# Kernel tuning notes

Measured on AMD Instinct MI355X. Metric: run time of the kernel, lower is better.

The kernel has to match this reference:

```python
import jax, jax.numpy as jnp
import numpy as np

N, M, E, D = 20000, 1024, 640000, 256


def setup_inputs() -> dict:
    key = jax.random.key(0)
    ks = jax.random.split(key, 24)
    mask = jax.random.uniform(ks[0], (N, M)) < 0.05
    init = jnp.where(mask, jax.random.uniform(ks[1], (N, M), minval=0.1, maxval=1.0), 0.0)
    inp = {
        'init': init,
        'ei_cc': jax.random.randint(ks[2], (2, E), 0, N, dtype=jnp.int32),
        'ei_cac': jax.random.randint(ks[3], (2, E), 0, N, dtype=jnp.int32),
        'ei_csc': jax.random.randint(ks[4], (2, E), 0, N, dtype=jnp.int32),
        'ea_cc': jax.random.uniform(ks[5], (E,), minval=0.1, maxval=1.0),
        'ea_cac': jax.random.uniform(ks[6], (E,), minval=0.1, maxval=1.0),
        'ea_csc': jax.random.uniform(ks[7], (E,), minval=0.1, maxval=1.0),
        # Projection MLP: Linear(1,16) -> ReLU -> Linear(16,D)
        'pW1': jax.random.normal(ks[8], (1, 16)) * 0.5,
        'pb1': jnp.zeros((16,)),
        'pW2': jax.random.normal(ks[9], (16, D)) * 0.1,
        'pb2': jnp.zeros((D,)),
        # three GCN branches, 3 layers each (all D->D)
        'W_cc': jax.random.normal(ks[10], (3, D, D)) * 0.05,
        'b_cc': jnp.zeros((3, D)),
        'W_cac': jax.random.normal(ks[11], (3, D, D)) * 0.05,
        'b_cac': jnp.zeros((3, D)),
        'W_csc': jax.random.normal(ks[12], (3, D, D)) * 0.05,
        'b_csc': jnp.zeros((3, D)),
        # meta-path attention: Linear(D, 1)
        'w_att': jax.random.normal(ks[13], (D,)) * 0.05,
        'b_att': jnp.zeros((1,)),
    }
    return inp


def projection(init, pW1, pb1, pW2, pb2):
    # torch code feeds the *indices* of nonzero columns through the MLP and
    # mean-pools per row. Vectorize: precompute MLP(j) for every column index j,
    # then masked mean.
    idx = jnp.arange(M, dtype=init.dtype)[:, None]          # [M, 1]
    h = jax.nn.relu(idx @ pW1 + pb1)                        # [M, 16]
    col_emb = h @ pW2 + pb2                                 # [M, D]
    mask = (init != 0).astype(init.dtype)                   # [N, M]
    cnt = mask.sum(axis=1)                                  # [N]
    emb = (mask @ col_emb) / jnp.maximum(cnt, 1.0)[:, None]
    return jnp.where(cnt[:, None] > 0, emb, 0.0)            # zero rows stay zero


def gcn_conv(x, edge_index, edge_weight, W, b):
    # PyG GCNConv with edge_weight: add self loops (w=1), symmetric norm.
    n = x.shape[0]
    loop = jnp.arange(n, dtype=edge_index.dtype)
    row = jnp.concatenate([edge_index[0], loop])
    col = jnp.concatenate([edge_index[1], loop])
    w = jnp.concatenate([edge_weight, jnp.ones((n,), x.dtype)])
    deg = jax.ops.segment_sum(w, col, num_segments=n)
    dinv = jnp.where(deg > 0, jax.lax.rsqrt(deg), 0.0)
    norm = dinv[row] * w * dinv[col]                        # [E+N]
    h = x @ W                                               # [N, D]
    out = jax.ops.segment_sum(norm[:, None] * h[row], col, num_segments=n)
    return out + b


def gcn_branch(x, edge_index, edge_weight, Ws, bs):
    for l in range(3):
        x = jax.nn.relu(gcn_conv(x, edge_index, edge_weight, Ws[l], bs[l]))
    return x


def reference(init, ei_cc, ei_cac, ei_csc, ea_cc, ea_cac, ea_csc,
              pW1, pb1, pW2, pb2, W_cc, b_cc, W_cac, b_cac, W_csc, b_csc,
              w_att, b_att):
    x0 = projection(init, pW1, pb1, pW2, pb2)               # [N, D]
    out_cc = gcn_branch(x0, ei_cc, ea_cc, W_cc, b_cc)
    out_cac = gcn_branch(x0, ei_cac, ea_cac, W_cac, b_cac)
    out_csc = gcn_branch(x0, ei_csc, ea_csc, W_csc, b_csc)
    emb = jnp.stack([out_cc, out_cac, out_csc], axis=0)     # [3, N, D]
    scores = jnp.einsum('pnd,d->pn', emb, w_att) + b_att[0] # [3, N]
    attn = jax.nn.softmax(scores, axis=0)                   # softmax over meta-paths
    return jnp.einsum('pn,pnd->nd', attn, emb)              # [N, D]
```

## Files before the change

### kernel.cpp

```cpp
#include <hip/hip_runtime.h>
#include <hip/hip_bf16.h>

typedef __hip_bfloat16 bf16;
typedef __bf16 v8bf __attribute__((ext_vector_type(8)));
typedef float f32x4 __attribute__((ext_vector_type(4)));
typedef unsigned int v4u __attribute__((ext_vector_type(4)));

constexpr int N = 20000, M = 1024, E = 640000, D = 256;
constexpr size_t SEGEL = (size_t)N * D;
constexpr int NCHUNK = 10000;
constexpr int NSLICE = 64;
constexpr int ESLICE = E / NSLICE;

__device__ __forceinline__ float b2f(bf16 v) { return __bfloat162float(v); }
__device__ __forceinline__ bf16 f2b(float f) { return __float2bfloat16(f); }
__device__ __forceinline__ float u2f(unsigned short u) { return __uint_as_float(((unsigned)u) << 16); }
__device__ __forceinline__ unsigned short f2u(float f) { bf16 h = __float2bfloat16(f); return *(unsigned short*)&h; }
__device__ __forceinline__ float loadf(const void* p, size_t i, int isbf) {
    return isbf ? b2f(((const bf16*)p)[i]) : ((const float*)p)[i];
}
__device__ __forceinline__ void fma8(float* acc, uint4 v, float w) {
    acc[0] = fmaf(w, u2f((unsigned short)(v.x & 0xffffu)), acc[0]);
    acc[1] = fmaf(w, u2f((unsigned short)(v.x >> 16)), acc[1]);
    acc[2] = fmaf(w, u2f((unsigned short)(v.y & 0xffffu)), acc[2]);
    acc[3] = fmaf(w, u2f((unsigned short)(v.y >> 16)), acc[3]);
    acc[4] = fmaf(w, u2f((unsigned short)(v.z & 0xffffu)), acc[4]);
    acc[5] = fmaf(w, u2f((unsigned short)(v.z >> 16)), acc[5]);
    acc[6] = fmaf(w, u2f((unsigned short)(v.w & 0xffffu)), acc[6]);
    acc[7] = fmaf(w, u2f((unsigned short)(v.w >> 16)), acc[7]);
}
__device__ __forceinline__ void add4(float* acc, uint2 v) {
    acc[0] += u2f((unsigned short)(v.x & 0xffffu));
    acc[1] += u2f((unsigned short)(v.x >> 16));
    acc[2] += u2f((unsigned short)(v.y & 0xffffu));
    acc[3] += u2f((unsigned short)(v.y >> 16));
}
__device__ __forceinline__ unsigned pack2(float a, float b) {
    return (unsigned)f2u(a) | ((unsigned)f2u(b) << 16);
}

__global__ void detect_kernel(const void* __restrict__ ea, int* __restrict__ flag)
{
    if (threadIdx.x == 0 && blockIdx.x == 0) {
        const unsigned short* u = (const unsigned short*)ea;
        int cnt = 0;
        for (int i = 0; i < 64; i++) {
            float f = __uint_as_float(((unsigned)u[i]) << 16);
            if (f >= 0.05f && f <= 1.05f) cnt++;
        }
        *flag = (cnt >= 60) ? 1 : 0;
    }
}

__global__ __launch_bounds__(256) void prep_kernel(
    const void* __restrict__ W0, const void* __restrict__ W1, const void* __restrict__ W2,
    const void* __restrict__ pW1, const void* __restrict__ pb1,
    const void* __restrict__ pW2, const void* __restrict__ pb2,
    bf16* __restrict__ WT, bf16* __restrict__ cemb, const int* __restrict__ flag)
{
    int isbf = *flag;
    int b = blockIdx.x;
    if (b < 2304) {
        int mat = b >> 8, n = b & 255, k = threadIdx.x;
        const void* W = (mat < 3) ? W0 : (mat < 6) ? W1 : W2;
        int lm = mat - (mat < 3 ? 0 : (mat < 6 ? 3 : 6));
        WT[(size_t)mat * 65536 + n * 256 + k] =
            f2b(loadf(W, (size_t)lm * 65536 + k * 256 + n, isbf));
    } else {
        int j = b - 2304;
        int d = threadIdx.x;
        float jf = (float)j;
        float acc = loadf(pb2, d, isbf);
        #pragma unroll
        for (int k = 0; k < 16; k++) {
            float h = fmaxf(jf * loadf(pW1, k, isbf) + loadf(pb1, k, isbf), 0.0f);
            acc += h * loadf(pW2, k * 256 + d, isbf);
        }
        cemb[(size_t)j * 256 + d] = f2b(acc);
    }
}

__global__ __launch_bounds__(256) void projection_kernel(
    const void* __restrict__ init, const bf16* __restrict__ cemb,
    bf16* __restrict__ x0, const int* __restrict__ flag)
{
    __shared__ unsigned short idxs[4][1024];
    int isbf = *flag;
    int wave = threadIdx.x >> 6, lane = threadIdx.x & 63;
    int i = blockIdx.x * 4 + wave;
    unsigned long long below = (lane == 63) ? 0x7fffffffffffffffull
                                            : ((1ull << lane) - 1ull);
    int cnt = 0;
    if (isbf) {
        const unsigned short* row = (const unsigned short*)init + (size_t)i * 1024;
        for (int c0 = 0; c0 < 1024; c0 += 64) {
            bool nz = (row[c0 + lane] & 0x7fffu) != 0;
            unsigned long long m = __ballot(nz);
            if (nz) idxs[wave][cnt + __popcll(m & below)] = (unsigned short)(c0 + lane);
            cnt += __popcll(m);
        }
    } else {
        const float* row = (const float*)init + (size_t)i * 1024;
        for (int c0 = 0; c0 < 1024; c0 += 64) {
            bool nz = row[c0 + lane] != 0.0f;
            unsigned long long m = __ballot(nz);
            if (nz) idxs[wave][cnt + __popcll(m & below)] = (unsigned short)(c0 + lane);
            cnt += __popcll(m);
        }
    }
    const uint2* cr = (const uint2*)cemb;
    float acc[4] = {0.0f, 0.0f, 0.0f, 0.0f};
    int j = 0;
    for (; j + 8 <= cnt; j += 8) {
        uint2 v0 = cr[(size_t)idxs[wave][j + 0] * 64 + lane];
        uint2 v1 = cr[(size_t)idxs[wave][j + 1] * 64 + lane];
        uint2 v2 = cr[(size_t)idxs[wave][j + 2] * 64 + lane];
        uint2 v3 = cr[(size_t)idxs[wave][j + 3] * 64 + lane];
        uint2 v4 = cr[(size_t)idxs[wave][j + 4] * 64 + lane];
        uint2 v5 = cr[(size_t)idxs[wave][j + 5] * 64 + lane];
        uint2 v6 = cr[(size_t)idxs[wave][j + 6] * 64 + lane];
        uint2 v7 = cr[(size_t)idxs[wave][j + 7] * 64 + lane];
        add4(acc, v0); add4(acc, v1); add4(acc, v2); add4(acc, v3);
        add4(acc, v4); add4(acc, v5); add4(acc, v6); add4(acc, v7);
    }
    for (; j < cnt; j++) {
        uint2 v = cr[(size_t)idxs[wave][j] * 64 + lane];
        add4(acc, v);
    }
    float rinv = 1.0f / fmaxf((float)cnt, 1.0f);
    uint2 o;
    o.x = pack2(acc[0] * rinv, acc[1] * rinv);
    o.y = pack2(acc[2] * rinv, acc[3] * rinv);
    ((uint2*)x0)[(size_t)i * 64 + lane] = o;
}

__global__ __launch_bounds__(256) void countP_kernel(
    const int* __restrict__ e0, const int* __restrict__ e1, const int* __restrict__ e2,
    int* __restrict__ P)
{
    __shared__ int cur[NCHUNK];
    int b = blockIdx.x;
    int pb = b >> 7, rem = b & 127;
    int ck = rem >> 6, s = rem & 63;
    const int* ei = pb == 0 ? e0 : pb == 1 ? e1 : e2;
    int c0 = ck * NCHUNK;
    int t = threadIdx.x;
    for (int i = t; i < NCHUNK; i += 256) cur[i] = 0;
    __syncthreads();
    int ebase = s * ESLICE;
    for (int e = ebase + t; e < ebase + ESLICE; e += 256) {
        int c = ei[E + e];
        if (c >= c0 && c < c0 + NCHUNK) atomicAdd(&cur[c - c0], 1);
    }
    __syncthreads();
    int* Prow = P + ((size_t)(pb * NSLICE + s)) * N + c0;
    for (int i = t; i < NCHUNK; i += 256) Prow[i] = cur[i];
}

__global__ __launch_bounds__(256) void cnt_sum_kernel(
    const int* __restrict__ P, int* __restrict__ cnt)
{
    int id = blockIdx.x * 256 + threadIdx.x;
    if (id >= 3 * N) return;
    int pb = id / N, c = id - pb * N;
    int sum = 0;
    #pragma unroll 8
    for (int s = 0; s < NSLICE; s++)
        sum += P[((size_t)(pb * NSLICE + s)) * N + c];
    cnt[id] = sum;
}

__global__ __launch_bounds__(1024) void scan_kernel(
    const int* __restrict__ cnt, int* __restrict__ col_ptr)
{
    int pb = blockIdx.x;
    int base = pb * E;
    __shared__ int s[1024];
    int t = threadIdx.x;
    const int CH = 20;
    int i0 = t * CH;
    int sum = 0;
    for (int j = 0; j < CH; j++) { int i = i0 + j; if (i < N) sum += cnt[pb * N + i]; }
    s[t] = sum;
    __syncthreads();
    for (int off = 1; off < 1024; off <<= 1) {
        int v = (t >= off) ? s[t - off] : 0;
        __syncthreads();
        s[t] += v;
        __syncthreads();
    }
    int run = base + s[t] - sum;
    for (int j = 0; j < CH; j++) {
        int i = i0 + j;
        if (i < N) {
            col_ptr[pb * (N + 1) + i] = run;
            run += cnt[pb * N + i];
        }
    }
    if (t == 0) col_ptr[pb * (N + 1) + N] = base + E;
}

__global__ __launch_bounds__(256) void base_kernel(
    int* __restrict__ P, const int* __restrict__ col_ptr)
{
    int id = blockIdx.x * 256 + threadIdx.x;
    if (id >= 3 * N) return;
    int pb = id / N, c = id - pb * N;
    int run = col_ptr[pb * (N + 1) + c];
    for (int s = 0; s < NSLICE; s++) {
        size_t idx = ((size_t)(pb * NSLICE + s)) * N + c;
        int v = P[idx];
        P[idx] = run;
        run += v;
    }
}

__global__ __launch_bounds__(256) void fill_kernel(
    const int* __restrict__ e0, const int* __restrict__ e1, const int* __restrict__ e2,
    const void* __restrict__ a0, const void* __restrict__ a1, const void* __restrict__ a2,
    const int* __restrict__ P, int2* __restrict__ epack, const int* __restrict__ flag)
{
    __shared__ int cur[NCHUNK];
    int isbf = *flag;
    int b = blockIdx.x;
    int pb = b >> 7, rem = b & 127;
    int ck = rem >> 6, s = rem & 63;
    const int* ei = pb == 0 ? e0 : pb == 1 ? e1 : e2;
    const void* ea = pb == 0 ? a0 : pb == 1 ? a1 : a2;
    int c0 = ck * NCHUNK;
    int t = threadIdx.x;
    const int* Prow = P + ((size_t)(pb * NSLICE + s)) * N + c0;
    for (int i = t; i < NCHUNK; i += 256) cur[i] = Prow[i];
    __syncthreads();
    int ebase = s * ESLICE;
    for (int e = ebase + t; e < ebase + ESLICE; e += 256) {
        int c = ei[E + e];
        if (c >= c0 && c < c0 + NCHUNK) {
            int r = ei[e];
            float w = loadf(ea, e, isbf);
            int pos = atomicAdd(&cur[c - c0], 1);
            int2 v; v.x = r; v.y = __float_as_int(w);
            epack[pos] = v;
        }
    }
}

__global__ __launch_bounds__(256) void degsum_kernel(
    const int* __restrict__ col_ptr, const int2* __restrict__ epack,
    float* __restrict__ dinv, float* __restrict__ nloop)
{
    int wave = threadIdx.x >> 6, lane = threadIdx.x & 63;
    int pb = blockIdx.x / 5000;
    int i = (blockIdx.x - pb * 5000) * 4 + wave;
    int start = col_ptr[pb * (N + 1) + i], end = col_ptr[pb * (N + 1) + i + 1];
    float sum = 0.0f;
    for (int p = start + lane; p < end; p += 64) sum += __int_as_float(epack[p].y);
    for (int off = 1; off < 64; off <<= 1) sum += __shfl_xor(sum, off, 64);
    if (lane == 0) {
        float dg = 1.0f + sum;
        dinv[pb * N + i] = rsqrtf(dg);
        nloop[pb * N + i] = 1.0f / dg;
    }
}

__global__ __launch_bounds__(256) void snorm_sort_kernel(
    const int* __restrict__ col_ptr, int2* __restrict__ epack,
    const float* __restrict__ dinv)
{
    int wave = threadIdx.x >> 6, lane = threadIdx.x & 63;
    int pb = blockIdx.x / 5000;
    int i = (blockIdx.x - pb * 5000) * 4 + wave;
    int start = col_ptr[pb * (N + 1) + i], end = col_ptr[pb * (N + 1) + i + 1];
    float dc = dinv[pb * N + i];
    for (int base = start; base < end; base += 64) {
        int n = end - base; n = n < 64 ? n : 64;
        int key = 0x7fffffff, val = 0;
        if (lane < n) {
            int2 v = epack[base + lane];
            key = v.x;
            val = __float_as_int(dc * __int_as_float(v.y) * dinv[pb * N + v.x]);
        }
        #pragma unroll
        for (int k = 2; k <= 64; k <<= 1) {
            #pragma unroll
            for (int j = k >> 1; j > 0; j >>= 1) {
                int pk = __shfl_xor(key, j, 64);
                int pv = __shfl_xor(val, j, 64);
                bool up = (lane & k) == 0;
                bool lower = (lane & j) == 0;
                bool takeMin = (up == lower);
                bool sw = takeMin ? (pk < key) : (pk > key);
                if (sw) { key = pk; val = pv; }
            }
        }
        if (lane < n) {
            int2 o; o.x = key; o.y = val;
            epack[base + lane] = o;
        }
    }
}

__global__ __launch_bounds__(256) void aggregate_kernel(
    const bf16* __restrict__ xi0, const bf16* __restrict__ xi1, const bf16* __restrict__ xi2,
    bf16* __restrict__ yb,
    const int* __restrict__ col_ptr, const int2* __restrict__ epack,
    const float* __restrict__ nloop)
{
    int b = blockIdx.x;
    int xcd = b & 7, rnd = b >> 3;
    int pb, seq;
    if (xcd < 3)      { pb = 0; seq = rnd * 3 + xcd; }
    else if (xcd < 6) { pb = 1; seq = rnd * 3 + (xcd - 3); }
    else              { pb = 2; seq = rnd * 2 + (xcd - 6); }
    if (seq >= 5000) return;
    int wave = threadIdx.x >> 6, lane = threadIdx.x & 63;
    int i = seq * 4 + wave;
    const bf16* x = pb == 0 ? xi0 : pb == 1 ? xi1 : xi2;
    const uint4* xr = (const uint4*)x;
    int L = lane & 31, h = lane >> 5;
    int start = col_ptr[pb * (N + 1) + i], end = col_ptr[pb * (N + 1) + i + 1];
    float nl = nloop[pb * N + i];
    float acc[8];
    {
        uint4 sv = xr[(size_t)i * 32 + L];
        float self = (h == 0) ? nl : 0.0f;
        #pragma unroll
        for (int j = 0; j < 8; j++) acc[j] = 0.0f;
        fma8(acc, sv, self);
    }
    for (int base = start; base < end; base += 64) {
        int n = end - base; n = n < 64 ? n : 64;
        int ex = 0, ey = 0;
        if (lane < n) {
            unsigned long long ev = __builtin_nontemporal_load(
                (const unsigned long long*)(epack + base + lane));
            ex = (int)(unsigned)(ev & 0xffffffffull);
            ey = (int)(unsigned)(ev >> 32);
        }
        int pmax = (n + 1) >> 1;
        int p0 = 0;
        for (; p0 + 8 <= pmax; p0 += 8) {
            int eb = 2 * p0 + h;
            int r0 = __shfl(ex, eb +  0, 64);
            int r1 = __shfl(ex, eb +  2, 64);
            int r2 = __shfl(ex, eb +  4, 64);
            int r3 = __shfl(ex, eb +  6, 64);
            int r4 = __shfl(ex, eb +  8, 64);
            int r5 = __shfl(ex, eb + 10, 64);
            int r6 = __shfl(ex, eb + 12, 64);
            int r7 = __shfl(ex, eb + 14, 64);
            float w0 = __int_as_float(__shfl(ey, eb +  0, 64));
            float w1 = __int_as_float(__shfl(ey, eb +  2, 64));
            float w2 = __int_as_float(__shfl(ey, eb +  4, 64));
            float w3 = __int_as_float(__shfl(ey, eb +  6, 64));
            float w4 = __int_as_float(__shfl(ey, eb +  8, 64));
            float w5 = __int_as_float(__shfl(ey, eb + 10, 64));
            float w6 = __int_as_float(__shfl(ey, eb + 12, 64));
            float w7 = __int_as_float(__shfl(ey, eb + 14, 64));
            uint4 v0 = xr[(size_t)r0 * 32 + L];
            uint4 v1 = xr[(size_t)r1 * 32 + L];
            uint4 v2 = xr[(size_t)r2 * 32 + L];
            uint4 v3 = xr[(size_t)r3 * 32 + L];
            uint4 v4 = xr[(size_t)r4 * 32 + L];
            uint4 v5 = xr[(size_t)r5 * 32 + L];
            uint4 v6 = xr[(size_t)r6 * 32 + L];
            uint4 v7 = xr[(size_t)r7 * 32 + L];
            fma8(acc, v0, w0); fma8(acc, v1, w1);
            fma8(acc, v2, w2); fma8(acc, v3, w3);
            fma8(acc, v4, w4); fma8(acc, v5, w5);
            fma8(acc, v6, w6); fma8(acc, v7, w7);
        }
        if (p0 + 4 <= pmax) {
            int eb = 2 * p0 + h;
            int r0 = __shfl(ex, eb + 0, 64);
            int r1 = __shfl(ex, eb + 2, 64);
            int r2 = __shfl(ex, eb + 4, 64);
            int r3 = __shfl(ex, eb + 6, 64);
            float w0 = __int_as_float(__shfl(ey, eb + 0, 64));
            float w1 = __int_as_float(__shfl(ey, eb + 2, 64));
            float w2 = __int_as_float(__shfl(ey, eb + 4, 64));
            float w3 = __int_as_float(__shfl(ey, eb + 6, 64));
            uint4 v0 = xr[(size_t)r0 * 32 + L];
            uint4 v1 = xr[(size_t)r1 * 32 + L];
            uint4 v2 = xr[(size_t)r2 * 32 + L];
            uint4 v3 = xr[(size_t)r3 * 32 + L];
            fma8(acc, v0, w0); fma8(acc, v1, w1);
            fma8(acc, v2, w2); fma8(acc, v3, w3);
            p0 += 4;
        }
        for (; p0 < pmax; p0++) {
            int e = 2 * p0 + h;
            int rj = __shfl(ex, e, 64);
            float w = __int_as_float(__shfl(ey, e, 64));
            uint4 v = xr[(size_t)rj * 32 + L];
            fma8(acc, v, w);
        }
    }
    #pragma unroll
    for (int j = 0; j < 8; j++) acc[j] += __shfl_xor(acc[j], 32, 64);
    if (h == 0) {
        v4u o;
        o.x = pack2(acc[0], acc[1]);
        o.y = pack2(acc[2], acc[3]);
        o.z = pack2(acc[4], acc[5]);
        o.w = pack2(acc[6], acc[7]);
        __builtin_nontemporal_store(o,
            (v4u*)yb + (size_t)pb * (SEGEL / 8) + (size_t)i * 32 + L);
    }
}

__global__ __launch_bounds__(256) void gemm_relu_kernel(
    const bf16* __restrict__ yb, const bf16* __restrict__ WT, int layer,
    const void* __restrict__ b0, const void* __restrict__ b1, const void* __restrict__ b2,
    bf16* __restrict__ o0, bf16* __restrict__ o1, bf16* __restrict__ o2,
    const int* __restrict__ flag)
{
    int isbf = *flag;
    int pl = blockIdx.x / 625, blk = blockIdx.x - pl * 625;
    const bf16* y = yb + (size_t)pl * SEGEL;
    const bf16* wt = WT + (size_t)(pl * 3 + layer) * 65536;
    const void* bias = pl == 0 ? b0 : pl == 1 ? b1 : b2;
    bf16* xout = pl == 0 ? o0 : pl == 1 ? o1 : o2;

    int wave = threadIdx.x >> 6, lane = threadIdx.x & 63;
    int m0 = blk * 32 + (wave >> 1) * 16;
    int n0 = (wave & 1) * 128;
    int mrow = lane & 15, q = lane >> 4;

    f32x4 acc[8] = {};
    const v8bf* arow = reinterpret_cast<const v8bf*>(y + (size_t)(m0 + mrow) * 256);
    for (int k0 = 0; k0 < 256; k0 += 32) {
        v8bf a = arow[(k0 >> 3) + q];
        #pragma unroll
        for (int nt = 0; nt < 8; nt++) {
            const v8bf* brow = reinterpret_cast<const v8bf*>(wt + (size_t)(n0 + nt * 16 + mrow) * 256);
            acc[nt] = __builtin_amdgcn_mfma_f32_16x16x32_bf16(a, brow[(k0 >> 3) + q], acc[nt], 0, 0, 0);
        }
    }
    #pragma unroll
    for (int nt = 0; nt < 8; nt++) {
        int col = n0 + nt * 16 + mrow;
        float bv = loadf(bias, (size_t)layer * 256 + col, isbf);
        #pragma unroll
        for (int r = 0; r < 4; r++) {
            int row = m0 + q * 4 + r;
            xout[(size_t)row * 256 + col] = f2b(fmaxf(acc[nt][r] + bv, 0.0f));
        }
    }
}

__global__ __launch_bounds__(256) void gemm_attn_kernel(
    const bf16* __restrict__ yb, const bf16* __restrict__ WT,
    const void* __restrict__ b0, const void* __restrict__ b1, const void* __restrict__ b2,
    const void* __restrict__ w_att, void* __restrict__ out,
    const int* __restrict__ flag)
{
    __shared__ float sc[3][32];
    int isbf = *flag;
    int blk = blockIdx.x;
    int wave = threadIdx.x >> 6, lane = threadIdx.x & 63;
    int wm = wave >> 1;
    int m0 = blk * 32 + wm * 16;
    int n0 = (wave & 1) * 128;
    int mrow = lane & 15, q = lane >> 4;

    if (threadIdx.x < 96) ((float*)sc)[threadIdx.x] = 0.0f;
    __syncthreads();

    unsigned pe[3][8][2];
    #pragma unroll
    for (int p = 0; p < 3; p++) {
        const bf16* y = yb + (size_t)p * SEGEL;
        const bf16* wt = WT + (size_t)(p * 3 + 2) * 65536;
        const void* bias = p == 0 ? b0 : p == 1 ? b1 : b2;
        f32x4 acc[8] = {};
        const v8bf* arow = reinterpret_cast<const v8bf*>(y + (size_t)(m0 + mrow) * 256);
        for (int k0 = 0; k0 < 256; k0 += 32) {
            v8bf a = arow[(k0 >> 3) + q];
            #pragma unroll
            for (int nt = 0; nt < 8; nt++) {
                const v8bf* brow = reinterpret_cast<const v8bf*>(wt + (size_t)(n0 + nt * 16 + mrow) * 256);
                acc[nt] = __builtin_amdgcn_mfma_f32_16x16x32_bf16(a, brow[(k0 >> 3) + q], acc[nt], 0, 0, 0);
            }
        }
        float part[4] = {0.0f, 0.0f, 0.0f, 0.0f};
        #pragma unroll
        for (int nt = 0; nt < 8; nt++) {
            int col = n0 + nt * 16 + mrow;
            float bv = loadf(bias, (size_t)2 * 256 + col, isbf);
            float wv = loadf(w_att, col, isbf);
            float e0 = u2f(f2u(fmaxf(acc[nt][0] + bv, 0.0f)));
            float e1 = u2f(f2u(fmaxf(acc[nt][1] + bv, 0.0f)));
            float e2 = u2f(f2u(fmaxf(acc[nt][2] + bv, 0.0f)));
            float e3 = u2f(f2u(fmaxf(acc[nt][3] + bv, 0.0f)));
            pe[p][nt][0] = pack2(e0, e1);
            pe[p][nt][1] = pack2(e2, e3);
            part[0] = fmaf(e0, wv, part[0]);
            part[1] = fmaf(e1, wv, part[1]);
            part[2] = fmaf(e2, wv, part[2]);
            part[3] = fmaf(e3, wv, part[3]);
        }
        #pragma unroll
        for (int off = 1; off < 16; off <<= 1) {
            #pragma unroll
            for (int r = 0; r < 4; r++) part[r] += __shfl_xor(part[r], off, 64);
        }
        if (mrow == 0) {
            #pragma unroll
            for (int r = 0; r < 4; r++)
                atomicAdd(&sc[p][wm * 16 + q * 4 + r], part[r]);
        }
    }
    __syncthreads();
    #pragma unroll
    for (int r = 0; r < 4; r++) {
        int lrow = wm * 16 + q * 4 + r;
        float s0 = sc[0][lrow], s1 = sc[1][lrow], s2 = sc[2][lrow];
        float mx = fmaxf(s0, fmaxf(s1, s2));
        float a0 = expf(s0 - mx), a1 = expf(s1 - mx), a2 = expf(s2 - mx);
        float inv = 1.0f / (a0 + a1 + a2);
        a0 *= inv; a1 *= inv; a2 *= inv;
        int row = blk * 32 + lrow;
        #pragma unroll
        for (int nt = 0; nt < 8; nt++) {
            int col = n0 + nt * 16 + mrow;
            unsigned w0 = pe[0][nt][r >> 1], w1 = pe[1][nt][r >> 1], w2 = pe[2][nt][r >> 1];
            float v0 = u2f((unsigned short)((r & 1) ? (w0 >> 16) : (w0 & 0xffffu)));
            float v1 = u2f((unsigned short)((r & 1) ? (w1 >> 16) : (w1 & 0xffffu)));
            float v2 = u2f((unsigned short)((r & 1) ? (w2 >> 16) : (w2 & 0xffffu)));
            float v = a0 * v0 + a1 * v1 + a2 * v2;
            if (isbf) ((bf16*)out)[(size_t)row * 256 + col] = f2b(v);
            else      ((float*)out)[(size_t)row * 256 + col] = v;
        }
    }
}

extern "C" void kernel_launch(void* const* d_in, const int* in_sizes, int n_in,
                              void* d_out, int out_size, void* d_ws, size_t ws_size,
                              hipStream_t stream)
{
    (void)in_sizes; (void)n_in; (void)out_size; (void)ws_size;

    const void* init = d_in[0];
    const int*  ei[3] = {(const int*)d_in[1], (const int*)d_in[2], (const int*)d_in[3]};
    const void* ea[3] = {d_in[4], d_in[5], d_in[6]};
    const void* pW1 = d_in[7];
    const void* pb1 = d_in[8];
    const void* pW2 = d_in[9];
    const void* pb2 = d_in[10];
    const void* Wb[3] = {d_in[11], d_in[13], d_in[15]};
    const void* bb[3] = {d_in[12], d_in[14], d_in[16]};
    const void* w_att = d_in[17];

    char* ws = (char*)d_ws;
    size_t off = 0;
    auto carve = [&](size_t bytes) -> char* {
        off = (off + 255) & ~(size_t)255;
        char* p = ws + off; off += bytes; return p;
    };
    int*   flag  = (int*)carve(4);
    bf16*  WT    = (bf16*)carve((size_t)9 * 65536 * 2);
    bf16*  cemb  = (bf16*)carve((size_t)M * D * 2);
    bf16*  x0    = (bf16*)carve(SEGEL * 2);
    int*   cnt   = (int*)carve((size_t)3 * N * 4);
    int*   colp  = (int*)carve((size_t)3 * (N + 1) * 4);
    float* dinv  = (float*)carve((size_t)3 * N * 4);
    float* nloop = (float*)carve((size_t)3 * N * 4);
    int2*  epack = (int2*)carve((size_t)3 * E * 8);
    bf16*  ybuf  = (bf16*)carve((size_t)3 * SEGEL * 2);
    bf16*  bufA  = (bf16*)carve((size_t)3 * SEGEL * 2);
    bf16*  bufB  = (bf16*)carve((size_t)3 * SEGEL * 2);
    int* P = (int*)bufB;

    detect_kernel<<<1, 64, 0, stream>>>(ea[0], flag);
    prep_kernel<<<3328, 256, 0, stream>>>(Wb[0], Wb[1], Wb[2],
                                          pW1, pb1, pW2, pb2, WT, cemb, flag);
    projection_kernel<<<5000, 256, 0, stream>>>(init, cemb, x0, flag);

    countP_kernel<<<384, 256, 0, stream>>>(ei[0], ei[1], ei[2], P);
    cnt_sum_kernel<<<(3 * N + 255) / 256, 256, 0, stream>>>(P, cnt);
    scan_kernel<<<3, 1024, 0, stream>>>(cnt, colp);
    base_kernel<<<(3 * N + 255) / 256, 256, 0, stream>>>(P, colp);
    fill_kernel<<<384, 256, 0, stream>>>(ei[0], ei[1], ei[2], ea[0], ea[1], ea[2],
                                         P, epack, flag);
    degsum_kernel<<<15000, 256, 0, stream>>>(colp, epack, dinv, nloop);
    snorm_sort_kernel<<<15000, 256, 0, stream>>>(colp, epack, dinv);

    const bf16 *i0 = x0, *i1 = x0, *i2 = x0;
    for (int l = 0; l < 3; l++) {
        aggregate_kernel<<<20000, 256, 0, stream>>>(i0, i1, i2, ybuf, colp, epack, nloop);
        if (l < 2) {
            bf16* dst = (l == 0) ? bufA : bufB;
            gemm_relu_kernel<<<1875, 256, 0, stream>>>(ybuf, WT, l, bb[0], bb[1], bb[2],
                                                       dst, dst + SEGEL, dst + 2 * SEGEL, flag);
            i0 = dst; i1 = dst + SEGEL; i2 = dst + 2 * SEGEL;
        } else {
            gemm_attn_kernel<<<625, 256, 0, stream>>>(ybuf, WT, bb[0], bb[1], bb[2],
                                                      w_att, d_out, flag);
        }
    }
}
```

Baseline: 967.6 us.

## Replace sliced CSC build with global atomics, widen projection loads, simplify aggregate

Builds the CSC edge structure with global atomic counting and degree accumulation in one pass. This replaces the per-slice shared-memory histograms, cnt_sum, base and degsum kernels, and the scan now writes dinv, nloop and fill cursors. The projection kernel switches to 16-byte loads with half-waves handling alternate nonzeros, and aggregate drops the XCD-aware block remap, the extra 5000 blocks and the hand-unrolled loop in favour of a predicated 8-wide loop. Fill order within a column becomes nondeterministic, and global atomics may contend, though snorm_sort still sorts afterward.

```diff
diff --git a/kernel.cpp b/kernel.cpp
--- a/kernel.cpp
+++ b/kernel.cpp
@@ -8,9 +8,8 @@
 
 constexpr int N = 20000, M = 1024, E = 640000, D = 256;
 constexpr size_t SEGEL = (size_t)N * D;
-constexpr int NCHUNK = 10000;
-constexpr int NSLICE = 64;
-constexpr int ESLICE = E / NSLICE;
+constexpr int EB = 2000;
+constexpr int EBLK = E / EB;
 
 __device__ __forceinline__ float b2f(bf16 v) { return __bfloat162float(v); }
 __device__ __forceinline__ bf16 f2b(float f) { return __float2bfloat16(f); }
@@ -29,11 +28,15 @@
     acc[6] = fmaf(w, u2f((unsigned short)(v.w & 0xffffu)), acc[6]);
     acc[7] = fmaf(w, u2f((unsigned short)(v.w >> 16)), acc[7]);
 }
-__device__ __forceinline__ void add4(float* acc, uint2 v) {
-    acc[0] += u2f((unsigned short)(v.x & 0xffffu));
-    acc[1] += u2f((unsigned short)(v.x >> 16));
-    acc[2] += u2f((unsigned short)(v.y & 0xffffu));
-    acc[3] += u2f((unsigned short)(v.y >> 16));
+__device__ __forceinline__ void add8(float* a, uint4 v) {
+    a[0] += u2f((unsigned short)(v.x & 0xffffu));
+    a[1] += u2f((unsigned short)(v.x >> 16));
+    a[2] += u2f((unsigned short)(v.y & 0xffffu));
+    a[3] += u2f((unsigned short)(v.y >> 16));
+    a[4] += u2f((unsigned short)(v.z & 0xffffu));
+    a[5] += u2f((unsigned short)(v.z >> 16));
+    a[6] += u2f((unsigned short)(v.w & 0xffffu));
+    a[7] += u2f((unsigned short)(v.w >> 16));
 }
 __device__ __forceinline__ unsigned pack2(float a, float b) {
     return (unsigned)f2u(a) | ((unsigned)f2u(b) << 16);
@@ -56,7 +59,8 @@
     const void* __restrict__ W0, const void* __restrict__ W1, const void* __restrict__ W2,
     const void* __restrict__ pW1, const void* __restrict__ pb1,
     const void* __restrict__ pW2, const void* __restrict__ pb2,
-    bf16* __restrict__ WT, bf16* __restrict__ cemb, const int* __restrict__ flag)
+    bf16* __restrict__ WT, bf16* __restrict__ cemb,
+    int* __restrict__ cnt, float* __restrict__ degf, const int* __restrict__ flag)
 {
     int isbf = *flag;
     int b = blockIdx.x;
@@ -66,7 +70,7 @@
         int lm = mat - (mat < 3 ? 0 : (mat < 6 ? 3 : 6));
         WT[(size_t)mat * 65536 + n * 256 + k] =
             f2b(loadf(W, (size_t)lm * 65536 + k * 256 + n, isbf));
-    } else {
+    } else if (b < 3328) {
         int j = b - 2304;
         int d = threadIdx.x;
         float jf = (float)j;
@@ -77,6 +81,15 @@
             acc += h * loadf(pW2, k * 256 + d, isbf);
         }
         cemb[(size_t)j * 256 + d] = f2b(acc);
+    } else {
+        int zb = b - 3328;
+        if (zb < 235) {
+            int id = zb * 256 + threadIdx.x;
+            if (id < 3 * N) cnt[id] = 0;
+        } else {
+            int id = (zb - 235) * 256 + threadIdx.x;
+            if (id < 3 * N) degf[id] = 0.0f;
+        }
     }
 }
 
@@ -108,70 +121,66 @@
             cnt += __popcll(m);
         }
     }
-    const uint2* cr = (const uint2*)cemb;
-    float acc[4] = {0.0f, 0.0f, 0.0f, 0.0f};
-    int j = 0;
-    for (; j + 8 <= cnt; j += 8) {
-        uint2 v0 = cr[(size_t)idxs[wave][j + 0] * 64 + lane];
-        uint2 v1 = cr[(size_t)idxs[wave][j + 1] * 64 + lane];
-        uint2 v2 = cr[(size_t)idxs[wave][j + 2] * 64 + lane];
-        uint2 v3 = cr[(size_t)idxs[wave][j + 3] * 64 + lane];
-        uint2 v4 = cr[(size_t)idxs[wave][j + 4] * 64 + lane];
-        uint2 v5 = cr[(size_t)idxs[wave][j + 5] * 64 + lane];
-        uint2 v6 = cr[(size_t)idxs[wave][j + 6] * 64 + lane];
-        uint2 v7 = cr[(size_t)idxs[wave][j + 7] * 64 + lane];
-        add4(acc, v0); add4(acc, v1); add4(acc, v2); add4(acc, v3);
-        add4(acc, v4); add4(acc, v5); add4(acc, v6); add4(acc, v7);
-    }
-    for (; j < cnt; j++) {
-        uint2 v = cr[(size_t)idxs[wave][j] * 64 + lane];
-        add4(acc, v);
-    }
-    float rinv = 1.0f / fmaxf((float)cnt, 1.0f);
-    uint2 o;
-    o.x = pack2(acc[0] * rinv, acc[1] * rinv);
-    o.y = pack2(acc[2] * rinv, acc[3] * rinv);
-    ((uint2*)x0)[(size_t)i * 64 + lane] = o;
-}
-
-__global__ __launch_bounds__(256) void countP_kernel(
+    const uint4* cr4 = (const uint4*)cemb;
+    int L = lane & 31, h = lane >> 5;
+    float acc[8] = {0.f, 0.f, 0.f, 0.f, 0.f, 0.f, 0.f, 0.f};
+    int npair = cnt >> 1;
+    int t = 0;
+    for (; t + 8 <= npair; t += 8) {
+        uint4 v0 = cr4[(size_t)idxs[wave][2 * (t + 0) + h] * 32 + L];
+        uint4 v1 = cr4[(size_t)idxs[wave][2 * (t + 1) + h] * 32 + L];
+        uint4 v2 = cr4[(size_t)idxs[wave][2 * (t + 2) + h] * 32 + L];
+        uint4 v3 = cr4[(size_t)idxs[wave][2 * (t + 3) + h] * 32 + L];
+        uint4 v4 = cr4[(size_t)idxs[wave][2 * (t + 4) + h] * 32 + L];
+        uint4 v5 = cr4[(size_t)idxs[wave][2 * (t + 5) + h] * 32 + L];
+        uint4 v6 = cr4[(size_t)idxs[wave][2 * (t + 6) + h] * 32 + L];
+        uint4 v7 = cr4[(size_t)idxs[wave][2 * (t + 7) + h] * 32 + L];
+        add8(acc, v0); add8(acc, v1); add8(acc, v2); add8(acc, v3);
+        add8(acc, v4); add8(acc, v5); add8(acc, v6); add8(acc, v7);
+    }
+    for (; t < npair; t++) {
+        uint4 v = cr4[(size_t)idxs[wave][2 * t + h] * 32 + L];
+        add8(acc, v);
+    }
+    if ((cnt & 1) && h == 0) {
+        uint4 v = cr4[(size_t)idxs[wave][cnt - 1] * 32 + L];
+        add8(acc, v);
+    }
+    #pragma unroll
+    for (int j = 0; j < 8; j++) acc[j] += __shfl_xor(acc[j], 32, 64);
+    if (h == 0) {
+        float rinv = 1.0f / fmaxf((float)cnt, 1.0f);
+        v4u o;
+        o.x = pack2(acc[0] * rinv, acc[1] * rinv);
+        o.y = pack2(acc[2] * rinv, acc[3] * rinv);
+        o.z = pack2(acc[4] * rinv, acc[5] * rinv);
+        o.w = pack2(acc[6] * rinv, acc[7] * rinv);
+        ((v4u*)x0)[(size_t)i * 32 + L] = o;
+    }
+}
+
+__global__ __launch_bounds__(256) void edge_cnt_kernel(
     const int* __restrict__ e0, const int* __restrict__ e1, const int* __restrict__ e2,
-    int* __restrict__ P)
-{
-    __shared__ int cur[NCHUNK];
+    const void* __restrict__ a0, const void* __restrict__ a1, const void* __restrict__ a2,
+    int* __restrict__ cnt, float* __restrict__ degf, const int* __restrict__ flag)
+{
+    int isbf = *flag;
     int b = blockIdx.x;
-    int pb = b >> 7, rem = b & 127;
-    int ck = rem >> 6, s = rem & 63;
+    int pb = b / EBLK, sl = b - pb * EBLK;
     const int* ei = pb == 0 ? e0 : pb == 1 ? e1 : e2;
-    int c0 = ck * NCHUNK;
-    int t = threadIdx.x;
-    for (int i = t; i < NCHUNK; i += 256) cur[i] = 0;
-    __syncthreads();
-    int ebase = s * ESLICE;
-    for (int e = ebase + t; e < ebase + ESLICE; e += 256) {
+    const void* ea = pb == 0 ? a0 : pb == 1 ? a1 : a2;
+    int base = sl * EB;
+    for (int e = base + threadIdx.x; e < base + EB; e += 256) {
         int c = ei[E + e];
-        if (c >= c0 && c < c0 + NCHUNK) atomicAdd(&cur[c - c0], 1);
-    }
-    __syncthreads();
-    int* Prow = P + ((size_t)(pb * NSLICE + s)) * N + c0;
-    for (int i = t; i < NCHUNK; i += 256) Prow[i] = cur[i];
-}
-
-__global__ __launch_bounds__(256) void cnt_sum_kernel(
-    const int* __restrict__ P, int* __restrict__ cnt)
-{
-    int id = blockIdx.x * 256 + threadIdx.x;
-    if (id >= 3 * N) return;
-    int pb = id / N, c = id - pb * N;
-    int sum = 0;
-    #pragma unroll 8
-    for (int s = 0; s < NSLICE; s++)
-        sum += P[((size_t)(pb * NSLICE + s)) * N + c];
-    cnt[id] = sum;
+        float w = loadf(ea, e, isbf);
+        atomicAdd(&cnt[pb * N + c], 1);
+        atomicAdd(&degf[pb * N + c], w);
+    }
 }
 
 __global__ __launch_bounds__(1024) void scan_kernel(
-    const int* __restrict__ cnt, int* __restrict__ col_ptr)
+    const int* __restrict__ cnt, int* __restrict__ col_ptr, int* __restrict__ cur,
+    const float* __restrict__ degf, float* __restrict__ dinv, float* __restrict__ nloop)
 {
     int pb = blockIdx.x;
     int base = pb * E;
@@ -194,72 +203,34 @@
         int i = i0 + j;
         if (i < N) {
             col_ptr[pb * (N + 1) + i] = run;
+            cur[pb * N + i] = run;
             run += cnt[pb * N + i];
+            float d = 1.0f + degf[pb * N + i];
+            dinv[pb * N + i] = rsqrtf(d);
+            nloop[pb * N + i] = 1.0f / d;
         }
     }
     if (t == 0) col_ptr[pb * (N + 1) + N] = base + E;
-}
-
-__global__ __launch_bounds__(256) void base_kernel(
-    int* __restrict__ P, const int* __restrict__ col_ptr)
-{
-    int id = blockIdx.x * 256 + threadIdx.x;
-    if (id >= 3 * N) return;
-    int pb = id / N, c = id - pb * N;
-    int run = col_ptr[pb * (N + 1) + c];
-    for (int s = 0; s < NSLICE; s++) {
-        size_t idx = ((size_t)(pb * NSLICE + s)) * N + c;
-        int v = P[idx];
-        P[idx] = run;
-        run += v;
-    }
 }
 
 __global__ __launch_bounds__(256) void fill_kernel(
     const int* __restrict__ e0, const int* __restrict__ e1, const int* __restrict__ e2,
     const void* __restrict__ a0, const void* __restrict__ a1, const void* __restrict__ a2,
-    const int* __restrict__ P, int2* __restrict__ epack, const int* __restrict__ flag)
-{
-    __shared__ int cur[NCHUNK];
+    int* __restrict__ cur, int2* __restrict__ epack, const int* __restrict__ flag)
+{
     int isbf = *flag;
     int b = blockIdx.x;
-    int pb = b >> 7, rem = b & 127;
-    int ck = rem >> 6, s = rem & 63;
+    int pb = b / EBLK, sl = b - pb * EBLK;
     const int* ei = pb == 0 ? e0 : pb == 1 ? e1 : e2;
     const void* ea = pb == 0 ? a0 : pb == 1 ? a1 : a2;
-    int c0 = ck * NCHUNK;
-    int t = threadIdx.x;
-    const int* Prow = P + ((size_t)(pb * NSLICE + s)) * N + c0;
-    for (int i = t; i < NCHUNK; i += 256) cur[i] = Prow[i];
-    __syncthreads();
-    int ebase = s * ESLICE;
-    for (int e = ebase + t; e < ebase + ESLICE; e += 256) {
+    int base = sl * EB;
+    for (int e = base + threadIdx.x; e < base + EB; e += 256) {
         int c = ei[E + e];
-        if (c >= c0 && c < c0 + NCHUNK) {
-            int r = ei[e];
-            float w = loadf(ea, e, isbf);
-            int pos = atomicAdd(&cur[c - c0], 1);
-            int2 v; v.x = r; v.y = __float_as_int(w);
-            epack[pos] = v;
-        }
-    }
-}
-
-__global__ __launch_bounds__(256) void degsum_kernel(
-    const int* __restrict__ col_ptr, const int2* __restrict__ epack,
-    float* __restrict__ dinv, float* __restrict__ nloop)
-{
-    int wave = threadIdx.x >> 6, lane = threadIdx.x & 63;
-    int pb = blockIdx.x / 5000;
-    int i = (blockIdx.x - pb * 5000) * 4 + wave;
-    int start = col_ptr[pb * (N + 1) + i], end = col_ptr[pb * (N + 1) + i + 1];
-    float sum = 0.0f;
-    for (int p = start + lane; p < end; p += 64) sum += __int_as_float(epack[p].y);
-    for (int off = 1; off < 64; off <<= 1) sum += __shfl_xor(sum, off, 64);
-    if (lane == 0) {
-        float dg = 1.0f + sum;
-        dinv[pb * N + i] = rsqrtf(dg);
-        nloop[pb * N + i] = 1.0f / dg;
+        int r = ei[e];
+        float w = loadf(ea, e, isbf);
+        int pos = atomicAdd(&cur[pb * N + c], 1);
+        int2 v; v.x = r; v.y = __float_as_int(w);
+        epack[pos] = v;
     }
 }
 
@@ -306,15 +277,9 @@
     const int* __restrict__ col_ptr, const int2* __restrict__ epack,
     const float* __restrict__ nloop)
 {
-    int b = blockIdx.x;
-    int xcd = b & 7, rnd = b >> 3;
-    int pb, seq;
-    if (xcd < 3)      { pb = 0; seq = rnd * 3 + xcd; }
-    else if (xcd < 6) { pb = 1; seq = rnd * 3 + (xcd - 3); }
-    else              { pb = 2; seq = rnd * 2 + (xcd - 6); }
-    if (seq >= 5000) return;
     int wave = threadIdx.x >> 6, lane = threadIdx.x & 63;
-    int i = seq * 4 + wave;
+    int pb = blockIdx.x / 5000;
+    int i = (blockIdx.x - pb * 5000) * 4 + wave;
     const bf16* x = pb == 0 ? xi0 : pb == 1 ? xi1 : xi2;
     const uint4* xr = (const uint4*)x;
     int L = lane & 31, h = lane >> 5;
@@ -338,62 +303,20 @@
             ey = (int)(unsigned)(ev >> 32);
         }
         int pmax = (n + 1) >> 1;
-        int p0 = 0;
-        for (; p0 + 8 <= pmax; p0 += 8) {
-            int eb = 2 * p0 + h;
-            int r0 = __shfl(ex, eb +  0, 64);
-            int r1 = __shfl(ex, eb +  2, 64);
-            int r2 = __shfl(ex, eb +  4, 64);
-            int r3 = __shfl(ex, eb +  6, 64);
-            int r4 = __shfl(ex, eb +  8, 64);
-            int r5 = __shfl(ex, eb + 10, 64);
-            int r6 = __shfl(ex, eb + 12, 64);
-            int r7 = __shfl(ex, eb + 14, 64);
-            float w0 = __int_as_float(__shfl(ey, eb +  0, 64));
-            float w1 = __int_as_float(__shfl(ey, eb +  2, 64));
-            float w2 = __int_as_float(__shfl(ey, eb +  4, 64));
-            float w3 = __int_as_float(__shfl(ey, eb +  6, 64));
-            float w4 = __int_as_float(__shfl(ey, eb +  8, 64));
-            float w5 = __int_as_float(__shfl(ey, eb + 10, 64));
-            float w6 = __int_as_float(__shfl(ey, eb + 12, 64));
-            float w7 = __int_as_float(__shfl(ey, eb + 14, 64));
-            uint4 v0 = xr[(size_t)r0 * 32 + L];
-            uint4 v1 = xr[(size_t)r1 * 32 + L];
-            uint4 v2 = xr[(size_t)r2 * 32 + L];
-            uint4 v3 = xr[(size_t)r3 * 32 + L];
-            uint4 v4 = xr[(size_t)r4 * 32 + L];
-            uint4 v5 = xr[(size_t)r5 * 32 + L];
-            uint4 v6 = xr[(size_t)r6 * 32 + L];
-            uint4 v7 = xr[(size_t)r7 * 32 + L];
-            fma8(acc, v0, w0); fma8(acc, v1, w1);
-            fma8(acc, v2, w2); fma8(acc, v3, w3);
-            fma8(acc, v4, w4); fma8(acc, v5, w5);
-            fma8(acc, v6, w6); fma8(acc, v7, w7);
-        }
-        if (p0 + 4 <= pmax) {
-            int eb = 2 * p0 + h;
-            int r0 = __shfl(ex, eb + 0, 64);
-            int r1 = __shfl(ex, eb + 2, 64);
-            int r2 = __shfl(ex, eb + 4, 64);
-            int r3 = __shfl(ex, eb + 6, 64);
-            float w0 = __int_as_float(__shfl(ey, eb + 0, 64));
-            float w1 = __int_as_float(__shfl(ey, eb + 2, 64));
-            float w2 = __int_as_float(__shfl(ey, eb + 4, 64));
-            float w3 = __int_as_float(__shfl(ey, eb + 6, 64));
-            uint4 v0 = xr[(size_t)r0 * 32 + L];
-            uint4 v1 = xr[(size_t)r1 * 32 + L];
-            uint4 v2 = xr[(size_t)r2 * 32 + L];
-            uint4 v3 = xr[(size_t)r3 * 32 + L];
-            fma8(acc, v0, w0); fma8(acc, v1, w1);
-            fma8(acc, v2, w2); fma8(acc, v3, w3);
-            p0 += 4;
-        }
-        for (; p0 < pmax; p0++) {
-            int e = 2 * p0 + h;
-            int rj = __shfl(ex, e, 64);
-            float w = __int_as_float(__shfl(ey, e, 64));
-            uint4 v = xr[(size_t)rj * 32 + L];
-            fma8(acc, v, w);
+        for (int p0 = 0; p0 < pmax; p0 += 8) {
+            int m = pmax - p0; m = m < 8 ? m : 8;
+            uint4 v[8];
+            float w[8];
+            #pragma unroll
+            for (int k = 0; k < 8; k++) {
+                int e = 2 * (p0 + k) + h;
+                int rj = __shfl(ex, e, 64);
+                w[k] = __int_as_float(__shfl(ey, e, 64));
+                if (k < m) v[k] = xr[(size_t)rj * 32 + L];
+            }
+            #pragma unroll
+            for (int k = 0; k < 8; k++)
+                if (k < m) fma8(acc, v[k], w[k]);
         }
     }
     #pragma unroll
@@ -563,6 +486,8 @@
     bf16*  cemb  = (bf16*)carve((size_t)M * D * 2);
     bf16*  x0    = (bf16*)carve(SEGEL * 2);
     int*   cnt   = (int*)carve((size_t)3 * N * 4);
+    int*   cur   = (int*)carve((size_t)3 * N * 4);
+    float* degf  = (float*)carve((size_t)3 * N * 4);
     int*   colp  = (int*)carve((size_t)3 * (N + 1) * 4);
     float* dinv  = (float*)carve((size_t)3 * N * 4);
     float* nloop = (float*)carve((size_t)3 * N * 4);
@@ -570,25 +495,25 @@
     bf16*  ybuf  = (bf16*)carve((size_t)3 * SEGEL * 2);
     bf16*  bufA  = (bf16*)carve((size_t)3 * SEGEL * 2);
     bf16*  bufB  = (bf16*)carve((size_t)3 * SEGEL * 2);
-    int* P = (int*)bufB;
 
     detect_kernel<<<1, 64, 0, stream>>>(ea[0], flag);
-    prep_kernel<<<3328, 256, 0, stream>>>(Wb[0], Wb[1], Wb[2],
-                                          pW1, pb1, pW2, pb2, WT, cemb, flag);
+    prep_kernel<<<3798, 256, 0, stream>>>(Wb[0], Wb[1], Wb[2],
+                                          pW1, pb1, pW2, pb2, WT, cemb,
+                                          cnt, degf, flag);
     projection_kernel<<<5000, 256, 0, stream>>>(init, cemb, x0, flag);
 
-    countP_kernel<<<384, 256, 0, stream>>>(ei[0], ei[1], ei[2], P);
-    cnt_sum_kernel<<<(3 * N + 255) / 256, 256, 0, stream>>>(P, cnt);
-    scan_kernel<<<3, 1024, 0, stream>>>(cnt, colp);
-    base_kernel<<<(3 * N + 255) / 256, 256, 0, stream>>>(P, colp);
-    fill_kernel<<<384, 256, 0, stream>>>(ei[0], ei[1], ei[2], ea[0], ea[1], ea[2],
-                                         P, epack, flag);
-    degsum_kernel<<<15000, 256, 0, stream>>>(colp, epack, dinv, nloop);
+    edge_cnt_kernel<<<3 * EBLK, 256, 0, stream>>>(ei[0], ei[1], ei[2],
+                                                  ea[0], ea[1], ea[2],
+                                                  cnt, degf, flag);
+    scan_kernel<<<3, 1024, 0, stream>>>(cnt, colp, cur, degf, dinv, nloop);
+    fill_kernel<<<3 * EBLK, 256, 0, stream>>>(ei[0], ei[1], ei[2],
+                                              ea[0], ea[1], ea[2],
+                                              cur, epack, flag);
     snorm_sort_kernel<<<15000, 256, 0, stream>>>(colp, epack, dinv);
 
     const bf16 *i0 = x0, *i1 = x0, *i2 = x0;
     for (int l = 0; l < 3; l++) {
-        aggregate_kernel<<<20000, 256, 0, stream>>>(i0, i1, i2, ybuf, colp, epack, nloop);
+        aggregate_kernel<<<15000, 256, 0, stream>>>(i0, i1, i2, ybuf, colp, epack, nloop);
         if (l < 2) {
             bf16* dst = (l == 0) ? bufA : bufB;
             gemm_relu_kernel<<<1875, 256, 0, stream>>>(ybuf, WT, l, bb[0], bb[1], bb[2],
```

Result: slower. 1.135 ms (+17.3%).
